# Performance work log

Hardware: AMD Instinct MI355X
Metric: run time of the kernel (lower is better)

The kernel has to match this reference:

```python
import jax, jax.numpy as jnp
import numpy as np

B, S, D, H, F = 4, 4096, 1024, 16, 4096
CAP = 0.125
ROPE_BASE = 10000.0


def setup_inputs() -> dict:
    key = jax.random.key(0)
    ks = jax.random.split(key, 9)
    scale = 0.02
    x = jax.random.normal(ks[0], (B, S, D), jnp.float32)
    causal = jnp.where(jnp.tril(jnp.ones((S, S), bool)), 0.0, -1e9).astype(jnp.float32)
    attention_mask = jnp.broadcast_to(causal[None, None], (B, 1, S, S))
    position_ids = jnp.broadcast_to(jnp.arange(S, dtype=jnp.int32), (B, S))
    return {
        "x": x,
        "attention_mask": attention_mask,
        "position_ids": position_ids,
        "router_w": jax.random.normal(ks[1], (D, 1), jnp.float32) * scale,
        "router_b": jnp.zeros((1,), jnp.float32),
        "wq": jax.random.normal(ks[2], (D, D), jnp.float32) * scale,
        "wk": jax.random.normal(ks[3], (D, D), jnp.float32) * scale,
        "wv": jax.random.normal(ks[4], (D, D), jnp.float32) * scale,
        "wo": jax.random.normal(ks[5], (D, D), jnp.float32) * scale,
        "w1": jax.random.normal(ks[6], (D, F), jnp.float32) * scale,
        "w2": jax.random.normal(ks[7], (F, D), jnp.float32) * scale,
        "ln1": jnp.ones((D,), jnp.float32),
        "ln2": jnp.ones((D,), jnp.float32),
    }


def rmsnorm(x, g):
    return x * jax.lax.rsqrt(jnp.mean(x * x, -1, keepdims=True) + 1e-6) * g


def rope(t, pos):
    # t: [b, h, n, hd], pos: [b, n]
    hd = t.shape[-1]
    inv = 1.0 / (ROPE_BASE ** (jnp.arange(0, hd, 2, dtype=jnp.float32) / hd))
    f = pos[:, None, :, None].astype(jnp.float32) * inv  # [b,1,n,hd/2]
    emb = jnp.concatenate([f, f], axis=-1)
    cos, sin = jnp.cos(emb), jnp.sin(emb)
    rot = jnp.concatenate([-t[..., hd // 2:], t[..., : hd // 2]], axis=-1)
    return t * cos + rot * sin


def reference(x, attention_mask, position_ids, router_w, router_b,
              wq, wk, wv, wo, w1, w2, ln1, ln2):
    b, s, d = x.shape
    hd = d // H
    # router
    weights = (x @ router_w)[..., 0] + router_b[0]  # [b,s]
    k = int(CAP * s)
    topv, topi = jax.lax.top_k(weights, k)
    thr = topv[:, -1]
    sel_mask = (weights > thr[:, None]).astype(x.dtype)  # selects k-1 tokens/row
    kc = k - 1
    sel_idx = jnp.sort(topi[:, :kc], axis=1)  # preserve sequence order, [b,kc]
    bidx = jnp.arange(b)[:, None]
    # gather selected tokens / positions / weights
    x_sel = x[bidx, sel_idx]                 # [b,kc,d]
    pos_sel = position_ids[bidx, sel_idx]    # [b,kc]
    w_sel = weights[bidx, sel_idx]           # [b,kc]
    m = attention_mask[:, 0]                 # [b,s,s]
    m_sel = m[bidx[:, :, None], sel_idx[:, :, None], sel_idx[:, None, :]]  # [b,kc,kc]
    # transformer block on selected tokens
    hn = rmsnorm(x_sel, ln1)

    def heads(t):
        return t.reshape(b, kc, H, hd).transpose(0, 2, 1, 3)

    q = rope(heads(hn @ wq), pos_sel)
    kk = rope(heads(hn @ wk), pos_sel)
    v = heads(hn @ wv)
    sc = jnp.einsum('bhqd,bhkd->bhqk', q, kk) / np.sqrt(hd).astype(np.float32)
    sc = sc + m_sel[:, None]
    a = jax.nn.softmax(sc, axis=-1)
    o = jnp.einsum('bhqk,bhkd->bhqd', a, v).transpose(0, 2, 1, 3).reshape(b, kc, d) @ wo
    x1 = x_sel + o
    x2 = x1 + jax.nn.gelu(rmsnorm(x1, ln2) @ w1) @ w2
    # weighted scatter back + residual passthrough for unselected tokens
    proc = x2 * w_sel[..., None]
    out = jnp.zeros_like(x).at[bidx, sel_idx].set(proc)
    return out + x * (1.0 - sel_mask)[..., None]
```

## Files before the change

### kernel.cpp

```cpp
#include <hip/hip_runtime.h>

typedef __bf16 bf16;
typedef __bf16 bf16x8 __attribute__((ext_vector_type(8)));
typedef __bf16 bf16x4 __attribute__((ext_vector_type(4)));
typedef float f32x4 __attribute__((ext_vector_type(4)));

#define B_ 4
#define S_ 4096
#define D_ 1024
#define H_ 16
#define HD_ 64
#define F_ 4096
#define KC 512
#define M_ (B_ * KC)

#define GLDS16(gp, lp)                                                        \
    __builtin_amdgcn_global_load_lds(                                         \
        (const __attribute__((address_space(1))) void*)(gp),                  \
        (__attribute__((address_space(3))) void*)(lp), 16, 0, 0)

__global__ __launch_bounds__(256) void transpose_cast_kernel(const float* __restrict__ in,
                                                             bf16* __restrict__ out, int R, int C) {
    __shared__ bf16 tile[32][33];
    int tx = threadIdx.x & 31, ty = threadIdx.x >> 5;
    int c0 = blockIdx.x * 32, r0 = blockIdx.y * 32;
    for (int k = 0; k < 4; k++)
        tile[ty + k * 8][tx] = (bf16)in[(size_t)(r0 + ty + k * 8) * C + c0 + tx];
    __syncthreads();
    for (int k = 0; k < 4; k++)
        out[(size_t)(c0 + ty + k * 8) * R + r0 + tx] = tile[tx][ty + k * 8];
}

__global__ __launch_bounds__(256) void router_kernel(const float* __restrict__ x,
                                                     const float* __restrict__ rw,
                                                     const float* __restrict__ rb,
                                                     float* __restrict__ weights) {
    int wv = threadIdx.x >> 6, lane = threadIdx.x & 63;
    int t = blockIdx.x * 4 + wv;
    const float* xr = x + (size_t)t * D_;
    float s = 0.f;
    for (int c = 0; c < 4; c++) {
        int off = c * 256 + lane * 4;
        float4 xv = *(const float4*)(xr + off);
        float4 wv4 = *(const float4*)(rw + off);
        s += xv.x * wv4.x + xv.y * wv4.y + xv.z * wv4.z + xv.w * wv4.w;
    }
    for (int m = 32; m; m >>= 1) s += __shfl_down(s, m);
    if (lane == 0) weights[t] = s + rb[0];
}

__global__ __launch_bounds__(1024) void topk_kernel(const float* __restrict__ weights,
                                                    int* __restrict__ sel_idx,
                                                    float* __restrict__ w_sel,
                                                    float* __restrict__ thr) {
    __shared__ unsigned ords[S_];
    __shared__ unsigned hist[16][256];
    __shared__ unsigned wscan[16];
    __shared__ unsigned found[2];
    int b = blockIdx.x, tid = threadIdx.x, wv = tid >> 6, lane = tid & 63;
    const float* wb = weights + (size_t)b * S_;
    for (int i = tid; i < S_; i += 1024) {
        unsigned bits = __float_as_uint(wb[i]);
        ords[i] = (bits & 0x80000000u) ? ~bits : (bits | 0x80000000u);
    }
    unsigned pref = 0, pmask = 0;
    int rank = 512;
    for (int level = 0; level < 4; level++) {
        int shift = 24 - level * 8;
        for (int i = tid; i < 16 * 256; i += 1024) (&hist[0][0])[i] = 0;
        __syncthreads();
        for (int i = tid; i < S_; i += 1024) {
            unsigned o = ords[i];
            if ((o & pmask) == pref) atomicAdd(&hist[wv][(o >> shift) & 255], 1u);
        }
        __syncthreads();
        unsigned val = 0, v = 0;
        if (tid < 256) {
            unsigned s = 0;
            for (int w = 0; w < 16; w++) s += hist[w][255 - tid];
            val = s;
            v = s;
            for (int d = 1; d < 64; d <<= 1) {
                unsigned u = __shfl_up(v, d);
                if (lane >= d) v += u;
            }
            if (lane == 63) wscan[wv] = v;
        }
        __syncthreads();
        if (tid < 256) {
            unsigned woff = 0;
            for (int w = 0; w < wv; w++) woff += wscan[w];
            unsigned C = v + woff;
            if (val > 0 && C >= (unsigned)rank && C - val < (unsigned)rank) {
                found[0] = 255 - (unsigned)tid;
                found[1] = C - val;
            }
        }
        __syncthreads();
        pref |= found[0] << shift;
        pmask |= 0xffu << shift;
        rank -= (int)found[1];
        __syncthreads();
    }
    unsigned T = pref;
    int need_eq = rank - 1;
    unsigned cnt = 0;
    int i0 = tid * 4;
    unsigned o4[4];
    for (int k = 0; k < 4; k++) {
        unsigned o = ords[i0 + k];
        o4[k] = o;
        cnt += (o > T) ? 1u : 0u;
        cnt += (o == T) ? 0x10000u : 0u;
    }
    unsigned v2 = cnt;
    for (int d = 1; d < 64; d <<= 1) {
        unsigned u = __shfl_up(v2, d);
        if (lane >= d) v2 += u;
    }
    if (lane == 63) wscan[wv] = v2;
    __syncthreads();
    unsigned woff2 = 0;
    for (int w = 0; w < wv; w++) woff2 += wscan[w];
    unsigned excl = woff2 + v2 - cnt;
    unsigned gbe = excl & 0xffffu, ebe = excl >> 16;
    for (int k = 0; k < 4; k++) {
        unsigned o = o4[k];
        bool gt = o > T, eq = (o == T);
        if (gt || (eq && ebe < (unsigned)need_eq)) {
            unsigned esel = (ebe < (unsigned)need_eq) ? ebe : (unsigned)need_eq;
            unsigned pos = gbe + esel;
            sel_idx[b * KC + pos] = i0 + k;
            w_sel[b * KC + pos] = wb[i0 + k];
        }
        gbe += gt ? 1u : 0u;
        ebe += eq ? 1u : 0u;
    }
    if (tid == 0) {
        unsigned bits = (T & 0x80000000u) ? (T & 0x7fffffffu) : ~T;
        thr[b] = __uint_as_float(bits);
        sel_idx[b * KC + 511] = 0;
        w_sel[b * KC + 511] = 0.0f;
    }
}

__global__ __launch_bounds__(256) void gather_norm_kernel(const float* __restrict__ x,
                                                          const int* __restrict__ sel_idx,
                                                          const float* __restrict__ ln1,
                                                          bf16* __restrict__ hn) {
    int r = blockIdx.x, b = r >> 9, j = r & (KC - 1);
    int tid = threadIdx.x;
    bf16* outr = hn + (size_t)r * D_;
    if (j == 511) {
        ((uint2*)outr)[tid] = make_uint2(0u, 0u);
        return;
    }
    int idx = sel_idx[r];
    const float* xr = x + ((size_t)b * S_ + idx) * D_;
    float4 xv = ((const float4*)xr)[tid];
    float v[4] = {xv.x, xv.y, xv.z, xv.w}, ss = 0.f;
    for (int i = 0; i < 4; i++) ss += v[i] * v[i];
    __shared__ float red[4];
    float t = ss;
    for (int m = 32; m; m >>= 1) t += __shfl_down(t, m);
    if ((tid & 63) == 0) red[tid >> 6] = t;
    __syncthreads();
    ss = red[0] + red[1] + red[2] + red[3];
    float scale = rsqrtf(ss * (1.0f / D_) + 1e-6f);
    float4 lv = ((const float4*)ln1)[tid];
    float lg[4] = {lv.x, lv.y, lv.z, lv.w};
    bf16x4 o;
    for (int i = 0; i < 4; i++) o[i] = (bf16)(v[i] * scale * lg[i]);
    ((bf16x4*)outr)[tid] = o;
}

template <bool GELU>
__global__ __launch_bounds__(256) void gemm_bt(const bf16* __restrict__ A,
                                               const bf16* __restrict__ B0,
                                               const bf16* __restrict__ B1,
                                               const bf16* __restrict__ B2,
                                               bf16* __restrict__ C, int K, int N, int mat_shift) {
    __shared__ bf16 As[2][128 * 32];
    __shared__ bf16 Bs[2][128 * 32];
    int tid = threadIdx.x;
    int m0 = blockIdx.y * 128, n0 = blockIdx.x * 128;
    int wave = tid >> 6, lane = tid & 63, quad = lane >> 4, l16 = lane & 15;
    int wm = (wave >> 1) * 64, wn = (wave & 1) * 64;
    int mat = n0 >> mat_shift;
    const bf16* bp = (mat == 0) ? B0 : ((mat == 1) ? B1 : B2);
    int nb = n0 - (mat << mat_shift);
    int r0 = tid >> 2, ko = (tid & 3) * 8;
    const bf16* a0 = A + (size_t)(m0 + r0) * K + ko;
    const bf16* a1 = A + (size_t)(m0 + r0 + 64) * K + ko;
    const bf16* bq0 = bp + (size_t)(nb + r0) * K + ko;
    const bf16* bq1 = bp + (size_t)(nb + r0 + 64) * K + ko;
    int nk = K >> 5;
    GLDS16(a0, &As[0][tid * 8]);
    GLDS16(a1, &As[0][2048 + tid * 8]);
    GLDS16(bq0, &Bs[0][tid * 8]);
    GLDS16(bq1, &Bs[0][2048 + tid * 8]);
    f32x4 acc[4][4] = {};
    for (int t = 0; t < nk; t++) {
        int cur = t & 1, nxt = cur ^ 1;
        if (t + 1 < nk) {
            int ks = (t + 1) << 5;
            GLDS16(a0 + ks, &As[nxt][tid * 8]);
            GLDS16(a1 + ks, &As[nxt][2048 + tid * 8]);
            GLDS16(bq0 + ks, &Bs[nxt][tid * 8]);
            GLDS16(bq1 + ks, &Bs[nxt][2048 + tid * 8]);
            asm volatile("s_waitcnt vmcnt(4)\n\ts_barrier" ::: "memory");
        } else {
            asm volatile("s_waitcnt vmcnt(0)\n\ts_barrier" ::: "memory");
        }
        const bf16* Ac = &As[cur][0];
        const bf16* Bc = &Bs[cur][0];
        bf16x8 af[4], bfr[4];
        for (int tt = 0; tt < 4; tt++)
            af[tt] = *(const bf16x8*)(Ac + (wm + tt * 16 + l16) * 32 + quad * 8);
        for (int tt = 0; tt < 4; tt++)
            bfr[tt] = *(const bf16x8*)(Bc + (wn + tt * 16 + l16) * 32 + quad * 8);
        for (int tm = 0; tm < 4; tm++)
            for (int tn = 0; tn < 4; tn++)
                acc[tm][tn] = __builtin_amdgcn_mfma_f32_16x16x32_bf16(af[tm], bfr[tn], acc[tm][tn], 0, 0, 0);
        asm volatile("s_barrier" ::: "memory");
    }
    for (int tm = 0; tm < 4; tm++)
        for (int tn = 0; tn < 4; tn++) {
            int col = n0 + wn + tn * 16 + l16;
            for (int r = 0; r < 4; r++) {
                int row = m0 + wm + tm * 16 + quad * 4 + r;
                float v = acc[tm][tn][r];
                if (GELU) {
                    float x3 = v * v * v;
                    v = 0.5f * v * (1.f + tanhf(0.7978845608028654f * (v + 0.044715f * x3)));
                }
                C[(size_t)row * N + col] = (bf16)v;
            }
        }
}

__global__ __launch_bounds__(256) void rope_prep_kernel(const bf16* __restrict__ qkv,
                                                        const int* __restrict__ sel_idx,
                                                        const int* __restrict__ pos_ids,
                                                        bf16* __restrict__ Qh, bf16* __restrict__ Kh,
                                                        bf16* __restrict__ VT) {
    int r = blockIdx.x, b = r >> 9, j = r & (KC - 1);
    int idx = sel_idx[r];
    float pos = (j < 511) ? (float)pos_ids[b * S_ + idx] : 0.f;
    int t = threadIdx.x, h = t >> 4, tl = t & 15;
    const bf16* row = qkv + (size_t)r * 3072;
    int bh = b * H_ + h;
    size_t qbase = ((size_t)bh * KC + j) * HD_;
    for (int dd = 0; dd < 4; dd++) {
        int d = tl * 4 + dd;
        int p = (d < 32) ? d : d - 32;
        float inv = expf(-0.28782313662425572f * (float)p);
        float f = pos * inv;
        float cs = cosf(f), sn = sinf(f);
        float qd = (float)row[h * HD_ + d];
        float qo = (d < 32) ? (float)row[h * HD_ + d + 32] : (float)row[h * HD_ + d - 32];
        float qrot = (d < 32) ? -qo : qo;
        Qh[qbase + d] = (bf16)(qd * cs + qrot * sn);
        float kd = (float)row[D_ + h * HD_ + d];
        float ko = (d < 32) ? (float)row[D_ + h * HD_ + d + 32] : (float)row[D_ + h * HD_ + d - 32];
        float krot = (d < 32) ? -ko : ko;
        Kh[qbase + d] = (bf16)(kd * cs + krot * sn);
        VT[((size_t)bh * HD_ + d) * KC + j] = row[2 * D_ + h * HD_ + d];
    }
}

__global__ __launch_bounds__(256) void attn_kernel(const bf16* __restrict__ Qh,
                                                   const bf16* __restrict__ Kh,
                                                   const bf16* __restrict__ VT,
                                                   bf16* __restrict__ O) {
    __shared__ bf16 Qs[64 * 72];
    __shared__ bf16 Ks[128 * 72];
    __shared__ bf16 Vts[64 * 136];
    __shared__ bf16 Ps[64 * 136];
    int bh = blockIdx.y, qt = blockIdx.x;
    int q_base = qt * 64;
    int tid = threadIdx.x, wave = tid >> 6, lane = tid & 63, quad = lane >> 4, l16 = lane & 15;
    const bf16* qg = Qh + ((size_t)bh * KC + q_base) * HD_;
    for (int i = 0; i < 2; i++) {
        int c = tid * 2 + i, row = c >> 3, ko = (c & 7) * 8;
        *(uint4*)(Qs + row * 72 + ko) = *(const uint4*)(qg + row * HD_ + ko);
    }
    f32x4 oacc[4] = {};
    float mrow[4], lrow[4];
    for (int r = 0; r < 4; r++) { mrow[r] = -1e30f; lrow[r] = 0.f; }
    int kt_max = (q_base + 63) >> 7;
    for (int kt = 0; kt <= kt_max; kt++) {
        __syncthreads();
        const bf16* kg = Kh + ((size_t)bh * KC + kt * 128) * HD_;
        for (int i = 0; i < 4; i++) {
            int c = tid * 4 + i, row = c >> 3, ko = (c & 7) * 8;
            *(uint4*)(Ks + row * 72 + ko) = *(const uint4*)(kg + row * HD_ + ko);
        }
        const bf16* vg = VT + (size_t)bh * HD_ * KC + kt * 128;
        for (int i = 0; i < 4; i++) {
            int c = tid * 4 + i, row = c >> 4, ko = (c & 15) * 8;
            *(uint4*)(Vts + row * 136 + ko) = *(const uint4*)(vg + (size_t)row * KC + ko);
        }
        __syncthreads();
        f32x4 sacc[8] = {};
        for (int kk = 0; kk < 2; kk++) {
            bf16x8 aq = *(const bf16x8*)(Qs + (wave * 16 + l16) * 72 + kk * 32 + quad * 8);
            for (int tn = 0; tn < 8; tn++) {
                bf16x8 bk = *(const bf16x8*)(Ks + (tn * 16 + l16) * 72 + kk * 32 + quad * 8);
                sacc[tn] = __builtin_amdgcn_mfma_f32_16x16x32_bf16(aq, bk, sacc[tn], 0, 0, 0);
            }
        }
        for (int r = 0; r < 4; r++) {
            int qi = q_base + wave * 16 + quad * 4 + r;
            float sv[8], mx = -1e30f;
            for (int tn = 0; tn < 8; tn++) {
                int kj = kt * 128 + tn * 16 + l16;
                float s = sacc[tn][r] * 0.125f;
                if (kj > qi) s = -1e30f;
                sv[tn] = s;
                mx = fmaxf(mx, s);
            }
            for (int m = 1; m < 16; m <<= 1) mx = fmaxf(mx, __shfl_xor(mx, m));
            float mnew = fmaxf(mrow[r], mx);
            float alpha = __expf(mrow[r] - mnew);
            float rs = 0.f;
            for (int tn = 0; tn < 8; tn++) {
                float pv = __expf(sv[tn] - mnew);
                rs += pv;
                Ps[(wave * 16 + quad * 4 + r) * 136 + tn * 16 + l16] = (bf16)pv;
            }
            for (int m = 1; m < 16; m <<= 1) rs += __shfl_xor(rs, m);
            lrow[r] = lrow[r] * alpha + rs;
            mrow[r] = mnew;
            for (int tn = 0; tn < 4; tn++) oacc[tn][r] *= alpha;
        }
        __syncthreads();
        for (int kk = 0; kk < 4; kk++) {
            bf16x8 ap = *(const bf16x8*)(Ps + (wave * 16 + l16) * 136 + kk * 32 + quad * 8);
            for (int tn = 0; tn < 4; tn++) {
                bf16x8 bv = *(const bf16x8*)(Vts + (tn * 16 + l16) * 136 + kk * 32 + quad * 8);
                oacc[tn] = __builtin_amdgcn_mfma_f32_16x16x32_bf16(ap, bv, oacc[tn], 0, 0, 0);
            }
        }
    }
    int b = bh >> 4, h = bh & 15;
    for (int tn = 0; tn < 4; tn++)
        for (int r = 0; r < 4; r++) {
            int rowg = b * KC + q_base + wave * 16 + quad * 4 + r;
            int col = h * HD_ + tn * 16 + l16;
            O[(size_t)rowg * D_ + col] = (bf16)(oacc[tn][r] / lrow[r]);
        }
}

__global__ __launch_bounds__(256) void x1norm_kernel(const float* __restrict__ x,
                                                     const bf16* __restrict__ wo_out,
                                                     const int* __restrict__ sel_idx,
                                                     const float* __restrict__ ln2,
                                                     bf16* __restrict__ h_in) {
    int r = blockIdx.x, b = r >> 9;
    int idx = sel_idx[r];
    int tid = threadIdx.x;
    const float* xr = x + ((size_t)b * S_ + idx) * D_;
    float4 xv = ((const float4*)xr)[tid];
    bf16x4 ov = ((const bf16x4*)(wo_out + (size_t)r * D_))[tid];
    float v[4] = {xv.x + (float)ov[0], xv.y + (float)ov[1], xv.z + (float)ov[2], xv.w + (float)ov[3]};
    float ss = 0.f;
    for (int i = 0; i < 4; i++) ss += v[i] * v[i];
    __shared__ float red[4];
    float t = ss;
    for (int m = 32; m; m >>= 1) t += __shfl_down(t, m);
    if ((tid & 63) == 0) red[tid >> 6] = t;
    __syncthreads();
    ss = red[0] + red[1] + red[2] + red[3];
    float scale = rsqrtf(ss * (1.0f / D_) + 1e-6f);
    float4 lv = ((const float4*)ln2)[tid];
    float lg[4] = {lv.x, lv.y, lv.z, lv.w};
    bf16x4 o;
    for (int i = 0; i < 4; i++) o[i] = (bf16)(v[i] * scale * lg[i]);
    ((bf16x4*)(h_in + (size_t)r * D_))[tid] = o;
}

__global__ __launch_bounds__(256) void fill_kernel(const float* __restrict__ x,
                                                   const float* __restrict__ weights,
                                                   const float* __restrict__ thr,
                                                   float* __restrict__ out) {
    int c = blockIdx.x * 256 + threadIdx.x;
    int t = c >> 8;
    int b = t >> 12;
    float w = weights[t];
    float4 xv = ((const float4*)x)[c];
    float4 z = {0.f, 0.f, 0.f, 0.f};
    ((float4*)out)[c] = (w > thr[b]) ? z : xv;
}

__global__ __launch_bounds__(256) void scatter_kernel(const float* __restrict__ x,
                                                      const bf16* __restrict__ wo_out,
                                                      const bf16* __restrict__ f2,
                                                      const int* __restrict__ sel_idx,
                                                      const float* __restrict__ w_sel,
                                                      float* __restrict__ out) {
    int r = blockIdx.x, b = r >> 9, j = r & (KC - 1);
    if (j == 511) return;
    int idx = sel_idx[r];
    float ws = w_sel[r];
    int tid = threadIdx.x;
    const float* xr = x + ((size_t)b * S_ + idx) * D_;
    float4 xv = ((const float4*)xr)[tid];
    bf16x4 wv = ((const bf16x4*)(wo_out + (size_t)r * D_))[tid];
    bf16x4 fv = ((const bf16x4*)(f2 + (size_t)r * D_))[tid];
    float* orow = out + ((size_t)b * S_ + idx) * D_;
    float4 prev = ((const float4*)orow)[tid];
    float4 res;
    res.x = ((xv.x + (float)wv[0]) + (float)fv[0]) * ws + prev.x;
    res.y = ((xv.y + (float)wv[1]) + (float)fv[1]) * ws + prev.y;
    res.z = ((xv.z + (float)wv[2]) + (float)fv[2]) * ws + prev.z;
    res.w = ((xv.w + (float)wv[3]) + (float)fv[3]) * ws + prev.w;
    ((float4*)orow)[tid] = res;
}

extern "C" void kernel_launch(void* const* d_in, const int* in_sizes, int n_in,
                              void* d_out, int out_size, void* d_ws, size_t ws_size,
                              hipStream_t stream) {
    const float* x = (const float*)d_in[0];
    const int* pos_ids = (const int*)d_in[2];
    const float* rw = (const float*)d_in[3];
    const float* rb = (const float*)d_in[4];
    const float* wq = (const float*)d_in[5];
    const float* wk = (const float*)d_in[6];
    const float* wv = (const float*)d_in[7];
    const float* wo = (const float*)d_in[8];
    const float* w1 = (const float*)d_in[9];
    const float* w2 = (const float*)d_in[10];
    const float* ln1 = (const float*)d_in[11];
    const float* ln2 = (const float*)d_in[12];
    float* out = (float*)d_out;
    (void)in_sizes; (void)n_in; (void)out_size;

    constexpr size_t MB = 1ull << 20;
    char* scr = (ws_size >= 88 * MB) ? (char*)d_ws : (char*)d_in[1];
    float* weights = (float*)(scr + 0);
    float* thr     = (float*)(scr + 0x10000);
    int*   sel     = (int*)  (scr + 0x14000);
    float* wsel    = (float*)(scr + 0x18000);
    bf16*  hn      = (bf16*) (scr + 1 * MB);
    bf16*  wqT     = (bf16*) (scr + 5 * MB);
    bf16*  wkT     = (bf16*) (scr + 7 * MB);
    bf16*  wvT     = (bf16*) (scr + 9 * MB);
    bf16*  qkv     = (bf16*) (scr + 11 * MB);
    bf16*  Qh      = (bf16*) (scr + 23 * MB);
    bf16*  Kh      = (bf16*) (scr + 27 * MB);
    bf16*  VT      = (bf16*) (scr + 31 * MB);
    bf16*  obuf    = (bf16*) (scr + 35 * MB);
    bf16*  woT     = (bf16*) (scr + 39 * MB);
    bf16*  wo_out  = (bf16*) (scr + 41 * MB);
    bf16*  h_in    = (bf16*) (scr + 45 * MB);
    bf16*  w1T     = (bf16*) (scr + 49 * MB);
    bf16*  h1      = (bf16*) (scr + 57 * MB);
    bf16*  w2T     = (bf16*) (scr + 73 * MB);
    bf16*  f2      = (bf16*) (scr + 81 * MB);

    router_kernel<<<dim3(B_ * S_ / 4), 256, 0, stream>>>(x, rw, rb, weights);
    topk_kernel<<<dim3(B_), 1024, 0, stream>>>(weights, sel, wsel, thr);
    gather_norm_kernel<<<dim3(M_), 256, 0, stream>>>(x, sel, ln1, hn);
    transpose_cast_kernel<<<dim3(32, 32), 256, 0, stream>>>(wq, wqT, D_, D_);
    transpose_cast_kernel<<<dim3(32, 32), 256, 0, stream>>>(wk, wkT, D_, D_);
    transpose_cast_kernel<<<dim3(32, 32), 256, 0, stream>>>(wv, wvT, D_, D_);
    gemm_bt<false><<<dim3(24, 16), 256, 0, stream>>>(hn, wqT, wkT, wvT, qkv, D_, 3 * D_, 10);
    rope_prep_kernel<<<dim3(M_), 256, 0, stream>>>(qkv, sel, pos_ids, Qh, Kh, VT);
    attn_kernel<<<dim3(8, B_ * H_), 256, 0, stream>>>(Qh, Kh, VT, obuf);
    transpose_cast_kernel<<<dim3(32, 32), 256, 0, stream>>>(wo, woT, D_, D_);
    gemm_bt<false><<<dim3(8, 16), 256, 0, stream>>>(obuf, woT, woT, woT, wo_out, D_, D_, 10);
    x1norm_kernel<<<dim3(M_), 256, 0, stream>>>(x, wo_out, sel, ln2, h_in);
    transpose_cast_kernel<<<dim3(128, 32), 256, 0, stream>>>(w1, w1T, D_, F_);
    gemm_bt<true><<<dim3(32, 16), 256, 0, stream>>>(h_in, w1T, w1T, w1T, h1, D_, F_, 12);
    transpose_cast_kernel<<<dim3(32, 128), 256, 0, stream>>>(w2, w2T, F_, D_);
    gemm_bt<false><<<dim3(8, 16), 256, 0, stream>>>(h1, w2T, w2T, w2T, f2, F_, D_, 10);
    fill_kernel<<<dim3(B_ * S_ * D_ / 4 / 256), 256, 0, stream>>>(x, weights, thr, out);
    scatter_kernel<<<dim3(M_), 256, 0, stream>>>(x, wo_out, f2, sel, wsel, out);
}
```

Before: 656.0 us.

## Fuse router and weight transposes, triple-buffer GEMM, fuse output fill and scatter

Merges the router and all six weight transpose-casts into one launch, and switches the GEMM to a three-stage LDS pipeline that prefetches two tiles ahead. The separate V-transpose buffer is dropped, so attention now transposes V from the qkv buffer into LDS itself. An inverse index map built in top-k lets a single output kernel write each row once, instead of a full fill pass followed by a read-modify-write scatter. This trades fewer launches and less global traffic for more LDS per GEMM block, which may lower occupancy, plus strided scalar LDS writes in attention.

```diff
diff --git a/kernel.cpp b/kernel.cpp
--- a/kernel.cpp
+++ b/kernel.cpp
@@ -19,11 +19,45 @@
         (const __attribute__((address_space(1))) void*)(gp),                  \
         (__attribute__((address_space(3))) void*)(lp), 16, 0, 0)
 
-__global__ __launch_bounds__(256) void transpose_cast_kernel(const float* __restrict__ in,
-                                                             bf16* __restrict__ out, int R, int C) {
+__global__ __launch_bounds__(256) void prep_kernel(const float* __restrict__ x,
+                                                   const float* __restrict__ rw,
+                                                   const float* __restrict__ rb,
+                                                   float* __restrict__ weights,
+                                                   const float* __restrict__ wq, bf16* __restrict__ wqT,
+                                                   const float* __restrict__ wk, bf16* __restrict__ wkT,
+                                                   const float* __restrict__ wv, bf16* __restrict__ wvT,
+                                                   const float* __restrict__ wo, bf16* __restrict__ woT,
+                                                   const float* __restrict__ w1, bf16* __restrict__ w1T,
+                                                   const float* __restrict__ w2, bf16* __restrict__ w2T) {
+    int bid = blockIdx.x;
+    if (bid < 4096) {
+        int wvv = threadIdx.x >> 6, lane = threadIdx.x & 63;
+        int t = bid * 4 + wvv;
+        const float* xr = x + (size_t)t * D_;
+        float s = 0.f;
+        for (int c = 0; c < 4; c++) {
+            int off = c * 256 + lane * 4;
+            float4 xv = *(const float4*)(xr + off);
+            float4 wv4 = *(const float4*)(rw + off);
+            s += xv.x * wv4.x + xv.y * wv4.y + xv.z * wv4.z + xv.w * wv4.w;
+        }
+        for (int m = 32; m; m >>= 1) s += __shfl_down(s, m);
+        if (lane == 0) weights[t] = s + rb[0];
+        return;
+    }
+    bid -= 4096;
+    const float* in;
+    bf16* out;
+    int C, R, bx, by;
+    if (bid < 1024)      { in = wq; out = wqT; C = 1024; R = 1024; bx = bid & 31; by = bid >> 5; }
+    else if (bid < 2048) { int t = bid - 1024; in = wk; out = wkT; C = 1024; R = 1024; bx = t & 31; by = t >> 5; }
+    else if (bid < 3072) { int t = bid - 2048; in = wv; out = wvT; C = 1024; R = 1024; bx = t & 31; by = t >> 5; }
+    else if (bid < 4096) { int t = bid - 3072; in = wo; out = woT; C = 1024; R = 1024; bx = t & 31; by = t >> 5; }
+    else if (bid < 8192) { int t = bid - 4096; in = w1; out = w1T; C = 4096; R = 1024; bx = t & 127; by = t >> 7; }
+    else                 { int t = bid - 8192; in = w2; out = w2T; C = 1024; R = 4096; bx = t & 31; by = t >> 5; }
     __shared__ bf16 tile[32][33];
     int tx = threadIdx.x & 31, ty = threadIdx.x >> 5;
-    int c0 = blockIdx.x * 32, r0 = blockIdx.y * 32;
+    int c0 = bx * 32, r0 = by * 32;
     for (int k = 0; k < 4; k++)
         tile[ty + k * 8][tx] = (bf16)in[(size_t)(r0 + ty + k * 8) * C + c0 + tx];
     __syncthreads();
@@ -31,28 +65,11 @@
         out[(size_t)(c0 + ty + k * 8) * R + r0 + tx] = tile[tx][ty + k * 8];
 }
 
-__global__ __launch_bounds__(256) void router_kernel(const float* __restrict__ x,
-                                                     const float* __restrict__ rw,
-                                                     const float* __restrict__ rb,
-                                                     float* __restrict__ weights) {
-    int wv = threadIdx.x >> 6, lane = threadIdx.x & 63;
-    int t = blockIdx.x * 4 + wv;
-    const float* xr = x + (size_t)t * D_;
-    float s = 0.f;
-    for (int c = 0; c < 4; c++) {
-        int off = c * 256 + lane * 4;
-        float4 xv = *(const float4*)(xr + off);
-        float4 wv4 = *(const float4*)(rw + off);
-        s += xv.x * wv4.x + xv.y * wv4.y + xv.z * wv4.z + xv.w * wv4.w;
-    }
-    for (int m = 32; m; m >>= 1) s += __shfl_down(s, m);
-    if (lane == 0) weights[t] = s + rb[0];
-}
-
 __global__ __launch_bounds__(1024) void topk_kernel(const float* __restrict__ weights,
                                                     int* __restrict__ sel_idx,
                                                     float* __restrict__ w_sel,
-                                                    float* __restrict__ thr) {
+                                                    float* __restrict__ thr,
+                                                    int* __restrict__ invmap) {
     __shared__ unsigned ords[S_];
     __shared__ unsigned hist[16][256];
     __shared__ unsigned wscan[16];
@@ -62,6 +79,7 @@
     for (int i = tid; i < S_; i += 1024) {
         unsigned bits = __float_as_uint(wb[i]);
         ords[i] = (bits & 0x80000000u) ? ~bits : (bits | 0x80000000u);
+        invmap[b * S_ + i] = -1;
     }
     unsigned pref = 0, pmask = 0;
     int rank = 512;
@@ -90,10 +108,10 @@
         if (tid < 256) {
             unsigned woff = 0;
             for (int w = 0; w < wv; w++) woff += wscan[w];
-            unsigned C = v + woff;
-            if (val > 0 && C >= (unsigned)rank && C - val < (unsigned)rank) {
+            unsigned Ccnt = v + woff;
+            if (val > 0 && Ccnt >= (unsigned)rank && Ccnt - val < (unsigned)rank) {
                 found[0] = 255 - (unsigned)tid;
-                found[1] = C - val;
+                found[1] = Ccnt - val;
             }
         }
         __syncthreads();
@@ -132,6 +150,7 @@
             unsigned pos = gbe + esel;
             sel_idx[b * KC + pos] = i0 + k;
             w_sel[b * KC + pos] = wb[i0 + k];
+            invmap[b * S_ + i0 + k] = (int)pos;
         }
         gbe += gt ? 1u : 0u;
         ebe += eq ? 1u : 0u;
@@ -180,8 +199,8 @@
                                                const bf16* __restrict__ B1,
                                                const bf16* __restrict__ B2,
                                                bf16* __restrict__ C, int K, int N, int mat_shift) {
-    __shared__ bf16 As[2][128 * 32];
-    __shared__ bf16 Bs[2][128 * 32];
+    __shared__ bf16 As[3][128 * 32];
+    __shared__ bf16 Bs[3][128 * 32];
     int tid = threadIdx.x;
     int m0 = blockIdx.y * 128, n0 = blockIdx.x * 128;
     int wave = tid >> 6, lane = tid & 63, quad = lane >> 4, l16 = lane & 15;
@@ -195,19 +214,23 @@
     const bf16* bq0 = bp + (size_t)(nb + r0) * K + ko;
     const bf16* bq1 = bp + (size_t)(nb + r0 + 64) * K + ko;
     int nk = K >> 5;
-    GLDS16(a0, &As[0][tid * 8]);
-    GLDS16(a1, &As[0][2048 + tid * 8]);
-    GLDS16(bq0, &Bs[0][tid * 8]);
-    GLDS16(bq1, &Bs[0][2048 + tid * 8]);
+#define STAGE_T(buf, kk)                                                      \
+    do {                                                                      \
+        int ks = (kk) << 5;                                                   \
+        GLDS16(a0 + ks, &As[buf][tid * 8]);                                   \
+        GLDS16(a1 + ks, &As[buf][2048 + tid * 8]);                            \
+        GLDS16(bq0 + ks, &Bs[buf][tid * 8]);                                  \
+        GLDS16(bq1 + ks, &Bs[buf][2048 + tid * 8]);                           \
+    } while (0)
+    STAGE_T(0, 0);
+    STAGE_T(1, 1);
     f32x4 acc[4][4] = {};
+    int cur = 0, pf = 2;
     for (int t = 0; t < nk; t++) {
-        int cur = t & 1, nxt = cur ^ 1;
-        if (t + 1 < nk) {
-            int ks = (t + 1) << 5;
-            GLDS16(a0 + ks, &As[nxt][tid * 8]);
-            GLDS16(a1 + ks, &As[nxt][2048 + tid * 8]);
-            GLDS16(bq0 + ks, &Bs[nxt][tid * 8]);
-            GLDS16(bq1 + ks, &Bs[nxt][2048 + tid * 8]);
+        if (t + 2 < nk) {
+            STAGE_T(pf, t + 2);
+            asm volatile("s_waitcnt vmcnt(8)\n\ts_barrier" ::: "memory");
+        } else if (t + 1 < nk) {
             asm volatile("s_waitcnt vmcnt(4)\n\ts_barrier" ::: "memory");
         } else {
             asm volatile("s_waitcnt vmcnt(0)\n\ts_barrier" ::: "memory");
@@ -223,7 +246,10 @@
             for (int tn = 0; tn < 4; tn++)
                 acc[tm][tn] = __builtin_amdgcn_mfma_f32_16x16x32_bf16(af[tm], bfr[tn], acc[tm][tn], 0, 0, 0);
         asm volatile("s_barrier" ::: "memory");
-    }
+        cur = (cur == 2) ? 0 : cur + 1;
+        pf = (pf == 2) ? 0 : pf + 1;
+    }
+#undef STAGE_T
     for (int tm = 0; tm < 4; tm++)
         for (int tn = 0; tn < 4; tn++) {
             int col = n0 + wn + tn * 16 + l16;
@@ -242,8 +268,7 @@
 __global__ __launch_bounds__(256) void rope_prep_kernel(const bf16* __restrict__ qkv,
                                                         const int* __restrict__ sel_idx,
                                                         const int* __restrict__ pos_ids,
-                                                        bf16* __restrict__ Qh, bf16* __restrict__ Kh,
-                                                        bf16* __restrict__ VT) {
+                                                        bf16* __restrict__ Qh, bf16* __restrict__ Kh) {
     int r = blockIdx.x, b = r >> 9, j = r & (KC - 1);
     int idx = sel_idx[r];
     float pos = (j < 511) ? (float)pos_ids[b * S_ + idx] : 0.f;
@@ -265,19 +290,19 @@
         float ko = (d < 32) ? (float)row[D_ + h * HD_ + d + 32] : (float)row[D_ + h * HD_ + d - 32];
         float krot = (d < 32) ? -ko : ko;
         Kh[qbase + d] = (bf16)(kd * cs + krot * sn);
-        VT[((size_t)bh * HD_ + d) * KC + j] = row[2 * D_ + h * HD_ + d];
     }
 }
 
 __global__ __launch_bounds__(256) void attn_kernel(const bf16* __restrict__ Qh,
                                                    const bf16* __restrict__ Kh,
-                                                   const bf16* __restrict__ VT,
+                                                   const bf16* __restrict__ qkv,
                                                    bf16* __restrict__ O) {
     __shared__ bf16 Qs[64 * 72];
     __shared__ bf16 Ks[128 * 72];
     __shared__ bf16 Vts[64 * 136];
     __shared__ bf16 Ps[64 * 136];
     int bh = blockIdx.y, qt = blockIdx.x;
+    int bb = bh >> 4, hh = bh & 15;
     int q_base = qt * 64;
     int tid = threadIdx.x, wave = tid >> 6, lane = tid & 63, quad = lane >> 4, l16 = lane & 15;
     const bf16* qg = Qh + ((size_t)bh * KC + q_base) * HD_;
@@ -296,10 +321,11 @@
             int c = tid * 4 + i, row = c >> 3, ko = (c & 7) * 8;
             *(uint4*)(Ks + row * 72 + ko) = *(const uint4*)(kg + row * HD_ + ko);
         }
-        const bf16* vg = VT + (size_t)bh * HD_ * KC + kt * 128;
-        for (int i = 0; i < 4; i++) {
-            int c = tid * 4 + i, row = c >> 4, ko = (c & 15) * 8;
-            *(uint4*)(Vts + row * 136 + ko) = *(const uint4*)(vg + (size_t)row * KC + ko);
+        const bf16* vbase = qkv + ((size_t)(bb * KC + kt * 128)) * 3072 + 2 * D_ + hh * HD_;
+        for (int p = 0; p < 4; p++) {
+            int jj = p * 32 + (tid >> 3), ko = (tid & 7) * 8;
+            bf16x8 vv = *(const bf16x8*)(vbase + (size_t)jj * 3072 + ko);
+            for (int e = 0; e < 8; e++) Vts[(ko + e) * 136 + jj] = vv[e];
         }
         __syncthreads();
         f32x4 sacc[8] = {};
@@ -343,11 +369,10 @@
             }
         }
     }
-    int b = bh >> 4, h = bh & 15;
     for (int tn = 0; tn < 4; tn++)
         for (int r = 0; r < 4; r++) {
-            int rowg = b * KC + q_base + wave * 16 + quad * 4 + r;
-            int col = h * HD_ + tn * 16 + l16;
+            int rowg = bb * KC + q_base + wave * 16 + quad * 4 + r;
+            int col = hh * HD_ + tn * 16 + l16;
             O[(size_t)rowg * D_ + col] = (bf16)(oacc[tn][r] / lrow[r]);
         }
 }
@@ -380,42 +405,35 @@
     ((bf16x4*)(h_in + (size_t)r * D_))[tid] = o;
 }
 
-__global__ __launch_bounds__(256) void fill_kernel(const float* __restrict__ x,
-                                                   const float* __restrict__ weights,
-                                                   const float* __restrict__ thr,
-                                                   float* __restrict__ out) {
-    int c = blockIdx.x * 256 + threadIdx.x;
-    int t = c >> 8;
+__global__ __launch_bounds__(256) void out_fused_kernel(const float* __restrict__ x,
+                                                        const bf16* __restrict__ wo_out,
+                                                        const bf16* __restrict__ f2,
+                                                        const int* __restrict__ invmap,
+                                                        const float* __restrict__ weights,
+                                                        const float* __restrict__ thr,
+                                                        const float* __restrict__ w_sel,
+                                                        float* __restrict__ out) {
+    int t = blockIdx.x;
     int b = t >> 12;
+    int tid = threadIdx.x;
     float w = weights[t];
-    float4 xv = ((const float4*)x)[c];
-    float4 z = {0.f, 0.f, 0.f, 0.f};
-    ((float4*)out)[c] = (w > thr[b]) ? z : xv;
-}
-
-__global__ __launch_bounds__(256) void scatter_kernel(const float* __restrict__ x,
-                                                      const bf16* __restrict__ wo_out,
-                                                      const bf16* __restrict__ f2,
-                                                      const int* __restrict__ sel_idx,
-                                                      const float* __restrict__ w_sel,
-                                                      float* __restrict__ out) {
-    int r = blockIdx.x, b = r >> 9, j = r & (KC - 1);
-    if (j == 511) return;
-    int idx = sel_idx[r];
-    float ws = w_sel[r];
-    int tid = threadIdx.x;
-    const float* xr = x + ((size_t)b * S_ + idx) * D_;
-    float4 xv = ((const float4*)xr)[tid];
-    bf16x4 wv = ((const bf16x4*)(wo_out + (size_t)r * D_))[tid];
-    bf16x4 fv = ((const bf16x4*)(f2 + (size_t)r * D_))[tid];
-    float* orow = out + ((size_t)b * S_ + idx) * D_;
-    float4 prev = ((const float4*)orow)[tid];
+    float th = thr[b];
+    float4 xv = ((const float4*)(x + (size_t)t * D_))[tid];
     float4 res;
-    res.x = ((xv.x + (float)wv[0]) + (float)fv[0]) * ws + prev.x;
-    res.y = ((xv.y + (float)wv[1]) + (float)fv[1]) * ws + prev.y;
-    res.z = ((xv.z + (float)wv[2]) + (float)fv[2]) * ws + prev.z;
-    res.w = ((xv.w + (float)wv[3]) + (float)fv[3]) * ws + prev.w;
-    ((float4*)orow)[tid] = res;
+    if (w > th) { res.x = 0.f; res.y = 0.f; res.z = 0.f; res.w = 0.f; }
+    else res = xv;
+    int j = invmap[t];
+    if (j >= 0) {
+        int r = b * KC + j;
+        bf16x4 wv = ((const bf16x4*)(wo_out + (size_t)r * D_))[tid];
+        bf16x4 fv = ((const bf16x4*)(f2 + (size_t)r * D_))[tid];
+        float ws = w_sel[r];
+        res.x += ((xv.x + (float)wv[0]) + (float)fv[0]) * ws;
+        res.y += ((xv.y + (float)wv[1]) + (float)fv[1]) * ws;
+        res.z += ((xv.z + (float)wv[2]) + (float)fv[2]) * ws;
+        res.w += ((xv.w + (float)wv[3]) + (float)fv[3]) * ws;
+    }
+    ((float4*)(out + (size_t)t * D_))[tid] = res;
 }
 
 extern "C" void kernel_launch(void* const* d_in, const int* in_sizes, int n_in,
@@ -442,6 +460,7 @@
     float* thr     = (float*)(scr + 0x10000);
     int*   sel     = (int*)  (scr + 0x14000);
     float* wsel    = (float*)(scr + 0x18000);
+    int*   invmap  = (int*)  (scr + 0x20000);
     bf16*  hn      = (bf16*) (scr + 1 * MB);
     bf16*  wqT     = (bf16*) (scr + 5 * MB);
     bf16*  wkT     = (bf16*) (scr + 7 * MB);
@@ -449,7 +468,6 @@
     bf16*  qkv     = (bf16*) (scr + 11 * MB);
     bf16*  Qh      = (bf16*) (scr + 23 * MB);
     bf16*  Kh      = (bf16*) (scr + 27 * MB);
-    bf16*  VT      = (bf16*) (scr + 31 * MB);
     bf16*  obuf    = (bf16*) (scr + 35 * MB);
     bf16*  woT     = (bf16*) (scr + 39 * MB);
     bf16*  wo_out  = (bf16*) (scr + 41 * MB);
@@ -459,22 +477,17 @@
     bf16*  w2T     = (bf16*) (scr + 73 * MB);
     bf16*  f2      = (bf16*) (scr + 81 * MB);
 
-    router_kernel<<<dim3(B_ * S_ / 4), 256, 0, stream>>>(x, rw, rb, weights);
-    topk_kernel<<<dim3(B_), 1024, 0, stream>>>(weights, sel, wsel, thr);
+    prep_kernel<<<dim3(16384), 256, 0, stream>>>(x, rw, rb, weights,
+                                                 wq, wqT, wk, wkT, wv, wvT,
+                                                 wo, woT, w1, w1T, w2, w2T);
+    topk_kernel<<<dim3(B_), 1024, 0, stream>>>(weights, sel, wsel, thr, invmap);
     gather_norm_kernel<<<dim3(M_), 256, 0, stream>>>(x, sel, ln1, hn);
-    transpose_cast_kernel<<<dim3(32, 32), 256, 0, stream>>>(wq, wqT, D_, D_);
-    transpose_cast_kernel<<<dim3(32, 32), 256, 0, stream>>>(wk, wkT, D_, D_);
-    transpose_cast_kernel<<<dim3(32, 32), 256, 0, stream>>>(wv, wvT, D_, D_);
     gemm_bt<false><<<dim3(24, 16), 256, 0, stream>>>(hn, wqT, wkT, wvT, qkv, D_, 3 * D_, 10);
-    rope_prep_kernel<<<dim3(M_), 256, 0, stream>>>(qkv, sel, pos_ids, Qh, Kh, VT);
-    attn_kernel<<<dim3(8, B_ * H_), 256, 0, stream>>>(Qh, Kh, VT, obuf);
-    transpose_cast_kernel<<<dim3(32, 32), 256, 0, stream>>>(wo, woT, D_, D_);
+    rope_prep_kernel<<<dim3(M_), 256, 0, stream>>>(qkv, sel, pos_ids, Qh, Kh);
+    attn_kernel<<<dim3(8, B_ * H_), 256, 0, stream>>>(Qh, Kh, qkv, obuf);
     gemm_bt<false><<<dim3(8, 16), 256, 0, stream>>>(obuf, woT, woT, woT, wo_out, D_, D_, 10);
     x1norm_kernel<<<dim3(M_), 256, 0, stream>>>(x, wo_out, sel, ln2, h_in);
-    transpose_cast_kernel<<<dim3(128, 32), 256, 0, stream>>>(w1, w1T, D_, F_);
     gemm_bt<true><<<dim3(32, 16), 256, 0, stream>>>(h_in, w1T, w1T, w1T, h1, D_, F_, 12);
-    transpose_cast_kernel<<<dim3(32, 128), 256, 0, stream>>>(w2, w2T, F_, D_);
     gemm_bt<false><<<dim3(8, 16), 256, 0, stream>>>(h1, w2T, w2T, w2T, f2, F_, D_, 10);
-    fill_kernel<<<dim3(B_ * S_ * D_ / 4 / 256), 256, 0, stream>>>(x, weights, thr, out);
-    scatter_kernel<<<dim3(M_), 256, 0, stream>>>(x, wo_out, f2, sel, wsel, out);
-}
+    out_fused_kernel<<<dim3(B_ * S_), 256, 0, stream>>>(x, wo_out, f2, invmap, weights, thr, wsel, out);
+}
```

Result: faster. 612.2 us (-6.7%).
